# Optimization experiments

Measured on AMD Instinct MI355X. Metric: run time of the kernel, lower is better.

Reference implementation:

```python
import jax, jax.numpy as jnp
import numpy as np

BN_EPS = 1e-5

def _conv1x1(x, W, b):
    # x: (B,C,H,W), W: (O,C) -> (B,O,H,W)
    return jnp.einsum('oc,bchw->bohw', W, x) + b[None, :, None, None]

def setup_inputs() -> dict:
    key = jax.random.key(0)
    ks = jax.random.split(key, 6)
    B, C, H, W = 4, 256, 64, 64
    cq = C // 8
    x  = jax.random.normal(ks[0], (B, C, H, W), jnp.float32)
    Wq = jax.random.normal(ks[1], (cq, C), jnp.float32) * (1.0 / np.sqrt(C))
    Wk = jax.random.normal(ks[2], (cq, C), jnp.float32) * (1.0 / np.sqrt(C))
    Wv = jax.random.normal(ks[3], (C, C), jnp.float32) * (1.0 / np.sqrt(C))
    Wo = jax.random.normal(ks[4], (C, C, 3, 3), jnp.float32) * (1.0 / np.sqrt(C * 9))
    return {
        'x': x,
        'Wq': Wq, 'bq': jnp.zeros((cq,), jnp.float32),
        'Wk': Wk, 'bk': jnp.zeros((cq,), jnp.float32),
        'Wv': Wv, 'bv': jnp.zeros((C,), jnp.float32),
        'Wo': Wo, 'bo': jnp.zeros((C,), jnp.float32),
        'bn_gamma': jnp.ones((C,), jnp.float32),
        'bn_beta':  jnp.zeros((C,), jnp.float32),
        'bn_mean':  jnp.zeros((C,), jnp.float32),
        'bn_var':   jnp.ones((C,), jnp.float32),
    }

def reference(x, Wq, bq, Wk, bk, Wv, bv, Wo, bo, bn_gamma, bn_beta, bn_mean, bn_var):
    B, C, H, W = x.shape
    cq = Wq.shape[0]
    N = H * W
    q = _conv1x1(x, Wq, bq).reshape(B, cq, N)   # (B,cq,N)
    k = _conv1x1(x, Wk, bk).reshape(B, cq, N)   # (B,cq,N)
    v = _conv1x1(x, Wv, bv).reshape(B, C, N)    # (B,C,N)
    scale = cq ** (-0.5)
    attn = jnp.einsum('bcn,bcm->bnm', q, k) * scale   # (B,N,N)
    attn = jax.nn.softmax(attn, axis=-1)
    out = jnp.einsum('bnm,bcm->bcn', attn, v).reshape(B, C, H, W)
    # conv_output: 3x3 conv + BN (inference stats) + ReLU
    out = jax.lax.conv_general_dilated(
        out, Wo, window_strides=(1, 1), padding=((1, 1), (1, 1)),
        dimension_numbers=('NCHW', 'OIHW', 'NCHW')) + bo[None, :, None, None]
    inv = bn_gamma * jax.lax.rsqrt(bn_var + BN_EPS)
    out = out * inv[None, :, None, None] + (bn_beta - bn_mean * inv)[None, :, None, None]
    out = jax.nn.relu(out)
    return out + x
```

## Files before the change

### kernel.cpp

```cpp
#include <hip/hip_runtime.h>
#include <hip/hip_bf16.h>
#include <math.h>

#define N_TOK 4096

typedef __attribute__((ext_vector_type(8))) short short8;
typedef __attribute__((ext_vector_type(4))) float f32x4;

#define MFMA16(a, b, c) __builtin_amdgcn_mfma_f32_16x16x32_bf16(a, b, c, 0, 0, 0)

__device__ inline unsigned pack_bf16x2(float a, float b) {
    __hip_bfloat16 ha = __float2bfloat16(a), hb = __float2bfloat16(b);
    unsigned short ua = *(unsigned short*)&ha, ub = *(unsigned short*)&hb;
    return (unsigned)ua | ((unsigned)ub << 16);
}

__device__ inline float bf2f(unsigned short u) {
    unsigned v = ((unsigned)u) << 16;
    union { unsigned u; float f; } cv; cv.u = v; return cv.f;
}

__device__ inline int swz4(int h, int row) { return (h ^ row ^ (row >> 2)) & 3; }

#define SCK 0.25506974748975505f

__global__ __launch_bounds__(256) void w_prep_kernel(
    const float* __restrict__ Wo, const float* __restrict__ Wq,
    const float* __restrict__ Wk, const float* __restrict__ Wv,
    __hip_bfloat16* __restrict__ Wt, __hip_bfloat16* __restrict__ Wqk,
    __hip_bfloat16* __restrict__ Wvb)
{
    int blk = blockIdx.x, t = threadIdx.x;
    if (blk < 256) {
        const float* src = &Wo[(size_t)(blk * 256 + t) * 9];
#pragma unroll
        for (int tap = 0; tap < 9; ++tap)
            Wt[(size_t)(tap * 256 + blk) * 256 + t] = __float2bfloat16(src[tap]);
    } else if (blk < 260) {
        int r0 = (blk - 256) * 64;
        for (int r = r0; r < r0 + 64; ++r)
            Wvb[r * 256 + t] = __float2bfloat16(Wv[r * 256 + t]);
    } else {
        for (int r = 0; r < 32; ++r) {
            Wqk[r * 256 + t]        = __float2bfloat16(Wq[r * 256 + t] * SCK);
            Wqk[(r + 32) * 256 + t] = __float2bfloat16(Wk[r * 256 + t]);
        }
    }
}

__global__ __launch_bounds__(256) void qkv_kernel(
    const float* __restrict__ x,
    const __hip_bfloat16* __restrict__ Wqk, const __hip_bfloat16* __restrict__ Wvb,
    const float* __restrict__ bq, const float* __restrict__ bk,
    const float* __restrict__ bv,
    __hip_bfloat16* __restrict__ qg, __hip_bfloat16* __restrict__ kg,
    __hip_bfloat16* __restrict__ vg)
{
    __shared__ __hip_bfloat16 tl[32][72];
    int blk = blockIdx.x;
    int b = blk >> 7, n0 = (blk & 127) * 32;
    int t = threadIdx.x, w = t >> 6, lane = t & 63;
    int l15 = lane & 15, l4 = lane >> 4;
    int ns = w & 1, mg = w >> 1;
    int n = n0 + ns * 16 + l15;

    const __hip_bfloat16* wrow[10];
#pragma unroll
    for (int mi = 0; mi < 10; ++mi) {
        int row = mg ? ((6 + mi) * 16 + l15)
                     : (mi < 4 ? (mi * 16 + l15) : 0);
        const __hip_bfloat16* base = mg ? Wvb : (mi < 4 ? Wqk : Wvb);
        if (!mg && mi >= 4) row = (mi - 4) * 16 + l15;
        wrow[mi] = &base[(size_t)row * 256];
    }

    f32x4 zf = {0.f, 0.f, 0.f, 0.f};
    f32x4 acc[10];
#pragma unroll
    for (int m = 0; m < 10; ++m) acc[m] = zf;

    for (int cc = 0; cc < 256; cc += 64) {
        __syncthreads();
#pragma unroll
        for (int rep = 0; rep < 2; ++rep) {
            int c = rep * 32 + (t >> 3);
            int n4 = (t & 7) * 4;
            float4 v4 = *(const float4*)&x[((size_t)(b * 256 + cc + c)) * N_TOK + n0 + n4];
            tl[n4 + 0][c] = __float2bfloat16(v4.x);
            tl[n4 + 1][c] = __float2bfloat16(v4.y);
            tl[n4 + 2][c] = __float2bfloat16(v4.z);
            tl[n4 + 3][c] = __float2bfloat16(v4.w);
        }
        __syncthreads();
#pragma unroll
        for (int kk = 0; kk < 2; ++kk) {
            int k0 = cc + kk * 32;
            short8 bfr = *(const short8*)&tl[ns * 16 + l15][kk * 32 + l4 * 8];
#pragma unroll
            for (int mi = 0; mi < 10; ++mi) {
                short8 af = *(const short8*)&wrow[mi][k0 + l4 * 8];
                acc[mi] = MFMA16(af, bfr, acc[mi]);
            }
        }
    }

    if (mg == 0) {
        f32x4 bq0 = *(const f32x4*)&bq[l4 * 4];
        f32x4 bq1 = *(const f32x4*)&bq[16 + l4 * 4];
        f32x4 bk0 = *(const f32x4*)&bk[l4 * 4];
        f32x4 bk1 = *(const f32x4*)&bk[16 + l4 * 4];
        size_t obase = (size_t)(b * N_TOK + n) * 32;
        uint2 u;
        u.x = pack_bf16x2(acc[0][0] + bq0[0] * SCK, acc[0][1] + bq0[1] * SCK);
        u.y = pack_bf16x2(acc[0][2] + bq0[2] * SCK, acc[0][3] + bq0[3] * SCK);
        *(uint2*)&qg[obase + l4 * 4] = u;
        u.x = pack_bf16x2(acc[1][0] + bq1[0] * SCK, acc[1][1] + bq1[1] * SCK);
        u.y = pack_bf16x2(acc[1][2] + bq1[2] * SCK, acc[1][3] + bq1[3] * SCK);
        *(uint2*)&qg[obase + 16 + l4 * 4] = u;
        u.x = pack_bf16x2(acc[2][0] + bk0[0], acc[2][1] + bk0[1]);
        u.y = pack_bf16x2(acc[2][2] + bk0[2], acc[2][3] + bk0[3]);
        *(uint2*)&kg[obase + l4 * 4] = u;
        u.x = pack_bf16x2(acc[3][0] + bk1[0], acc[3][1] + bk1[1]);
        u.y = pack_bf16x2(acc[3][2] + bk1[2], acc[3][3] + bk1[3]);
        *(uint2*)&kg[obase + 16 + l4 * 4] = u;
#pragma unroll
        for (int mi = 4; mi < 10; ++mi) {
            int cb = (mi - 4) * 16 + l4 * 4;
            f32x4 bvv = *(const f32x4*)&bv[cb];
#pragma unroll
            for (int r = 0; r < 4; ++r)
                vg[((size_t)(b * 256 + cb + r)) * N_TOK + n] = __float2bfloat16(acc[mi][r] + bvv[r]);
        }
    } else {
#pragma unroll
        for (int mi = 0; mi < 10; ++mi) {
            int cb = (6 + mi) * 16 + l4 * 4;
            f32x4 bvv = *(const f32x4*)&bv[cb];
#pragma unroll
            for (int r = 0; r < 4; ++r)
                vg[((size_t)(b * 256 + cb + r)) * N_TOK + n] = __float2bfloat16(acc[mi][r] + bvv[r]);
        }
    }
}

__global__ __launch_bounds__(256, 2) void flash_kernel(
    const __hip_bfloat16* __restrict__ qg, const __hip_bfloat16* __restrict__ kg,
    const __hip_bfloat16* __restrict__ vg,
    __hip_bfloat16* __restrict__ ph0, __hip_bfloat16* __restrict__ ph1,
    float* __restrict__ Lh)
{
    __shared__ __hip_bfloat16 v_lds[2][128 * 64];
    __shared__ __hip_bfloat16 k_lds[2][64 * 32];
    __shared__ __hip_bfloat16 p_lds[4][32 * 64];

    int blk = blockIdx.x;
    int work = (blk & 7) * 64 + (blk >> 3);
    int g = work >> 6;
    int kh = g >> 2, cs = (g >> 1) & 1, bl = g & 1;
    int rem = work & 63;
    int b = ((rem >> 5) << 1) | bl;
    int qgp = rem & 31;
    int t = threadIdx.x, w = t >> 6, lane = t & 63;
    int l15 = lane & 15, l4 = lane >> 4;
    int qw = qgp * 128 + w * 32;

    short8 qf[2];
#pragma unroll
    for (int qs = 0; qs < 2; ++qs)
        qf[qs] = *(const short8*)&qg[((size_t)(b * N_TOK + qw + qs * 16 + l15)) * 32 + l4 * 8];

    f32x4 zf = {0.f, 0.f, 0.f, 0.f};
    f32x4 acc[2][8];
#pragma unroll
    for (int qs = 0; qs < 2; ++qs)
#pragma unroll
        for (int ct = 0; ct < 8; ++ct) acc[qs][ct] = zf;
    float Lr[2] = {0.f, 0.f};

    int vc  = t >> 1;
    int kb4 = (t & 1) * 4;
    int kr  = t >> 2;
    int kch = t & 3;

    const __hip_bfloat16* vrow  = &vg[((size_t)(b * 256 + cs * 128 + vc)) * N_TOK + kh * 2048];
    const __hip_bfloat16* kbase = &kg[((size_t)(b * N_TOK + kh * 2048)) * 32];

    uint4 vp[4], kp;

#pragma unroll
    for (int j = 0; j < 4; ++j)
        vp[j] = *(const uint4*)&vrow[(kb4 + j) * 8];
    kp = *(const uint4*)&kbase[kr * 32 + kch * 8];
#pragma unroll
    for (int j = 0; j < 4; ++j)
        *(uint4*)&v_lds[0][vc * 64 + (((2 * (kb4 + j)) ^ (vc & 14)) << 2)] = vp[j];
    *(uint4*)&k_lds[0][kr * 32 + swz4(kch, kr) * 8] = kp;
    __syncthreads();

    int buf = 0;
    for (int it = 0; it < 32; ++it) {
        int nm0 = it * 64 + 64;
        bool more = (it < 31);
        if (more) {
#pragma unroll
            for (int j = 0; j < 4; ++j)
                vp[j] = *(const uint4*)&vrow[nm0 + (kb4 + j) * 8];
            kp = *(const uint4*)&kbase[(size_t)(nm0 + kr) * 32 + kch * 8];
        }

        short8 kf[4];
#pragma unroll
        for (int kt = 0; kt < 4; ++kt) {
            int row = kt * 16 + l15;
            kf[kt] = *(const short8*)&k_lds[buf][row * 32 + swz4(l4, row) * 8];
        }
        f32x4 sf[2][4];
#pragma unroll
        for (int qs = 0; qs < 2; ++qs)
#pragma unroll
            for (int kt = 0; kt < 4; ++kt)
                sf[qs][kt] = MFMA16(kf[kt], qf[qs], zf);

#pragma unroll
        for (int qs = 0; qs < 2; ++qs) {
            int prow = qs * 16 + l15;
#pragma unroll
            for (int kt = 0; kt < 4; ++kt) {
                float p0 = exp2f(sf[qs][kt][0]);
                float p1 = exp2f(sf[qs][kt][1]);
                float p2 = exp2f(sf[qs][kt][2]);
                float p3 = exp2f(sf[qs][kt][3]);
                Lr[qs] += (p0 + p1) + (p2 + p3);
                uint2 u;
                u.x = pack_bf16x2(p0, p1);
                u.y = pack_bf16x2(p2, p3);
                *(uint2*)&p_lds[w][prow * 64 + (((kt * 4 + l4) ^ (l15 & 14)) << 2)] = u;
            }
        }

#pragma unroll
        for (int ks = 0; ks < 2; ++ks) {
            short8 pb[2];
#pragma unroll
            for (int qs = 0; qs < 2; ++qs)
                pb[qs] = *(const short8*)&p_lds[w][(qs * 16 + l15) * 64 +
                         (((ks * 8 + l4 * 2) ^ (l15 & 14)) << 2)];
#pragma unroll
            for (int ct = 0; ct < 8; ++ct) {
                int cr = ct * 16 + l15;
                short8 vf = *(const short8*)&v_lds[buf][cr * 64 +
                           (((ks * 8 + l4 * 2) ^ (cr & 14)) << 2)];
                acc[0][ct] = MFMA16(vf, pb[0], acc[0][ct]);
                acc[1][ct] = MFMA16(vf, pb[1], acc[1][ct]);
            }
        }

        if (more) {
#pragma unroll
            for (int j = 0; j < 4; ++j)
                *(uint4*)&v_lds[buf ^ 1][vc * 64 + (((2 * (kb4 + j)) ^ (vc & 14)) << 2)] = vp[j];
            *(uint4*)&k_lds[buf ^ 1][kr * 32 + swz4(kch, kr) * 8] = kp;
            buf ^= 1;
        }
        __syncthreads();
    }

#pragma unroll
    for (int qs = 0; qs < 2; ++qs) {
        float L = Lr[qs];
        L += __shfl_xor(L, 16);
        L += __shfl_xor(L, 32);
        int nq = qw + qs * 16 + l15;
        if (cs == 0 && l4 == 0)
            Lh[kh * 16384 + b * 4096 + nq] = L;
        __hip_bfloat16* pdst = kh ? ph1 : ph0;
        size_t pix = (size_t)(b * N_TOK + nq);
#pragma unroll
        for (int ct = 0; ct < 8; ++ct) {
            int cl = cs * 128 + ct * 16 + l4 * 4;
            uint2 u;
            u.x = pack_bf16x2(acc[qs][ct][0], acc[qs][ct][1]);
            u.y = pack_bf16x2(acc[qs][ct][2], acc[qs][ct][3]);
            *(uint2*)&pdst[pix * 256 + cl] = u;
        }
    }
}

__global__ __launch_bounds__(256) void conv_mfma_kernel(
    const __hip_bfloat16* __restrict__ ph0, const __hip_bfloat16* __restrict__ ph1,
    const float* __restrict__ Lh, const __hip_bfloat16* __restrict__ Wt,
    const float* __restrict__ bo,  const float* __restrict__ gamma,
    const float* __restrict__ beta, const float* __restrict__ mean,
    const float* __restrict__ var, const float* __restrict__ x,
    float* __restrict__ out)
{
    __shared__ __hip_bfloat16 in_lds[180 * 32];
    __shared__ __hip_bfloat16 wt_lds[9 * 64 * 32];

    int blk = blockIdx.x;
    int sp = blk & 31, ob = (blk >> 5) & 3, b = blk >> 7;
    int y0 = (sp >> 2) * 8, x0 = (sp & 3) * 16;
    int o0 = ob * 64;
    int t = threadIdx.x;
    int w = t >> 6, lane = t & 63;
    int l15 = lane & 15, l4 = lane >> 4;

    f32x4 zf = {0.f, 0.f, 0.f, 0.f};
    f32x4 acc[4][2];
#pragma unroll
    for (int m = 0; m < 4; ++m)
#pragma unroll
        for (int n = 0; n < 2; ++n) acc[m][n] = zf;

    for (int cc = 0; cc < 256; cc += 32) {
        __syncthreads();
        for (int jj = t; jj < 720; jj += 256) {
            int pix = jj >> 2, h = jj & 3;
            int iy = pix / 18, ix = pix - iy * 18;
            int gy = y0 - 1 + iy, gx = x0 - 1 + ix;
            uint4 val = {0u, 0u, 0u, 0u};
            if (gy >= 0 && gy < 64 && gx >= 0 && gx < 64) {
                int bn = b * 4096 + gy * 64 + gx;
                float inv = 1.f / (Lh[bn] + Lh[16384 + bn]);
                size_t e = (size_t)bn * 256 + cc + h * 8;
                uint4 a  = *(const uint4*)&ph0[e];
                uint4 b4 = *(const uint4*)&ph1[e];
                const unsigned* ap = (const unsigned*)&a;
                const unsigned* bp = (const unsigned*)&b4;
                unsigned* vpn = (unsigned*)&val;
#pragma unroll
                for (int j = 0; j < 4; ++j) {
                    float lo = (bf2f((unsigned short)(ap[j] & 0xffff)) +
                                bf2f((unsigned short)(bp[j] & 0xffff))) * inv;
                    float hi = (bf2f((unsigned short)(ap[j] >> 16)) +
                                bf2f((unsigned short)(bp[j] >> 16))) * inv;
                    vpn[j] = pack_bf16x2(lo, hi);
                }
            }
            *(uint4*)&in_lds[pix * 32 + swz4(h, pix) * 8] = val;
        }
        for (int jj = t; jj < 2304; jj += 256) {
            int tap = jj >> 8, rem = jj & 255;
            int o = rem >> 2, h = rem & 3;
            uint4 wv = *(const uint4*)&Wt[((size_t)(tap * 256 + o0 + o)) * 256 + cc + h * 8];
            *(uint4*)&wt_lds[tap * 2048 + o * 32 + swz4(h, o) * 8] = wv;
        }
        __syncthreads();

#pragma unroll
        for (int ky = 0; ky < 3; ++ky) {
#pragma unroll
            for (int kx = 0; kx < 3; ++kx) {
                int tap = ky * 3 + kx;
                short8 af[4];
#pragma unroll
                for (int m = 0; m < 4; ++m) {
                    int orow = m * 16 + l15;
                    af[m] = *(const short8*)&wt_lds[tap * 2048 + orow * 32 + swz4(l4, orow) * 8];
                }
#pragma unroll
                for (int ntw = 0; ntw < 2; ++ntw) {
                    int yy = w * 2 + ntw;
                    int p = (yy + ky) * 18 + kx + l15;
                    short8 bfr = *(const short8*)&in_lds[p * 32 + swz4(l4, p) * 8];
#pragma unroll
                    for (int m = 0; m < 4; ++m)
                        acc[m][ntw] = MFMA16(af[m], bfr, acc[m][ntw]);
                }
            }
        }
    }

#pragma unroll
    for (int m = 0; m < 4; ++m) {
#pragma unroll
        for (int r = 0; r < 4; ++r) {
            int oc = o0 + m * 16 + l4 * 4 + r;
            float inv = gamma[oc] * rsqrtf(var[oc] + 1e-5f);
            float sh  = (bo[oc] - mean[oc]) * inv + beta[oc];
#pragma unroll
            for (int ntw = 0; ntw < 2; ++ntw) {
                int gy = y0 + w * 2 + ntw, gx = x0 + l15;
                size_t idx = (size_t)(b * 256 + oc) * 4096 + (size_t)gy * 64 + gx;
                float yv = acc[m][ntw][r] * inv + sh;
                yv = fmaxf(yv, 0.f);
                out[idx] = yv + x[idx];
            }
        }
    }
}

extern "C" void kernel_launch(void* const* d_in, const int* in_sizes, int n_in,
                              void* d_out, int out_size, void* d_ws, size_t ws_size,
                              hipStream_t stream)
{
    const float* x  = (const float*)d_in[0];
    const float* Wq = (const float*)d_in[1];
    const float* bq = (const float*)d_in[2];
    const float* Wk = (const float*)d_in[3];
    const float* bk = (const float*)d_in[4];
    const float* Wv = (const float*)d_in[5];
    const float* bv = (const float*)d_in[6];
    const float* Wo = (const float*)d_in[7];
    const float* bo = (const float*)d_in[8];
    const float* gm = (const float*)d_in[9];
    const float* bt = (const float*)d_in[10];
    const float* mn = (const float*)d_in[11];
    const float* vr = (const float*)d_in[12];
    float* out = (float*)d_out;

    char* wsb = (char*)d_ws;
    __hip_bfloat16* qg  = (__hip_bfloat16*)(wsb);
    __hip_bfloat16* kg  = (__hip_bfloat16*)(wsb + (1u  << 20));
    __hip_bfloat16* vg  = (__hip_bfloat16*)(wsb + (2u  << 20));
    __hip_bfloat16* ph1 = (__hip_bfloat16*)(wsb + (10u << 20));
    __hip_bfloat16* Wt  = (__hip_bfloat16*)(wsb + (18u << 20));
    __hip_bfloat16* ph0 = (__hip_bfloat16*)(wsb + (20u << 20));
    __hip_bfloat16* Wqk = (__hip_bfloat16*)(wsb + (28u << 20));
    __hip_bfloat16* Wvb = (__hip_bfloat16*)(wsb + (28u << 20) + 65536);
    float*          Lh  = (float*)(wsb + (28u << 20) + 262144);

    w_prep_kernel  <<<261,  256, 0, stream>>>(Wo, Wq, Wk, Wv, Wt, Wqk, Wvb);
    qkv_kernel     <<<512,  256, 0, stream>>>(x, Wqk, Wvb, bq, bk, bv, qg, kg, vg);
    flash_kernel   <<<512,  256, 0, stream>>>(qg, kg, vg, ph0, ph1, Lh);
    conv_mfma_kernel<<<512, 256, 0, stream>>>(ph0, ph1, Lh, Wt, bo, gm, bt, mn, vr, x, out);
}
```

Measured before the change: 150.0 us.

## Split flash KV range into three chunks and load K fragments directly

The flash attention grid grows from two KV halves to three uneven KV chunks (22/21/21 tiles), giving 768 blocks instead of 512 to spread work more evenly across CUs. K fragments are now loaded from global memory straight into MFMA registers, prefetched one tile ahead, instead of being staged through LDS, which drops the k_lds buffer. The conv kernel then merges three bf16 partial outputs and three row sums, adding a third partial buffer and extra memory traffic in exchange.

```diff
diff --git a/kernel.cpp b/kernel.cpp
--- a/kernel.cpp
+++ b/kernel.cpp
@@ -147,19 +147,18 @@
     const __hip_bfloat16* __restrict__ qg, const __hip_bfloat16* __restrict__ kg,
     const __hip_bfloat16* __restrict__ vg,
     __hip_bfloat16* __restrict__ ph0, __hip_bfloat16* __restrict__ ph1,
-    float* __restrict__ Lh)
+    __hip_bfloat16* __restrict__ ph2, float* __restrict__ Lh)
 {
     __shared__ __hip_bfloat16 v_lds[2][128 * 64];
-    __shared__ __hip_bfloat16 k_lds[2][64 * 32];
     __shared__ __hip_bfloat16 p_lds[4][32 * 64];
 
     int blk = blockIdx.x;
-    int work = (blk & 7) * 64 + (blk >> 3);
-    int g = work >> 6;
-    int kh = g >> 2, cs = (g >> 1) & 1, bl = g & 1;
-    int rem = work & 63;
-    int b = ((rem >> 5) << 1) | bl;
-    int qgp = rem & 31;
+    int work = (blk & 7) * 96 + (blk >> 3);
+    int kh = work >> 8;
+    int rem = work & 255;
+    int cs = rem >> 7, b = (rem >> 5) & 3, qgp = rem & 31;
+    int koff  = (kh == 0) ? 0 : (kh == 1 ? 1408 : 2752);
+    int iters = (kh == 0) ? 22 : 21;
     int t = threadIdx.x, w = t >> 6, lane = t & 63;
     int l15 = lane & 15, l4 = lane >> 4;
     int qw = qgp * 128 + w * 32;
@@ -179,47 +178,43 @@
 
     int vc  = t >> 1;
     int kb4 = (t & 1) * 4;
-    int kr  = t >> 2;
-    int kch = t & 3;
-
-    const __hip_bfloat16* vrow  = &vg[((size_t)(b * 256 + cs * 128 + vc)) * N_TOK + kh * 2048];
-    const __hip_bfloat16* kbase = &kg[((size_t)(b * N_TOK + kh * 2048)) * 32];
-
-    uint4 vp[4], kp;
+
+    const __hip_bfloat16* vrow  = &vg[((size_t)(b * 256 + cs * 128 + vc)) * N_TOK + koff];
+    const __hip_bfloat16* kbase = &kg[((size_t)(b * N_TOK + koff)) * 32];
+
+    uint4 vp[4];
+    short8 kfr[4], kfn[4];
 
 #pragma unroll
     for (int j = 0; j < 4; ++j)
         vp[j] = *(const uint4*)&vrow[(kb4 + j) * 8];
-    kp = *(const uint4*)&kbase[kr * 32 + kch * 8];
+#pragma unroll
+    for (int kt = 0; kt < 4; ++kt)
+        kfr[kt] = *(const short8*)&kbase[(kt * 16 + l15) * 32 + l4 * 8];
 #pragma unroll
     for (int j = 0; j < 4; ++j)
         *(uint4*)&v_lds[0][vc * 64 + (((2 * (kb4 + j)) ^ (vc & 14)) << 2)] = vp[j];
-    *(uint4*)&k_lds[0][kr * 32 + swz4(kch, kr) * 8] = kp;
     __syncthreads();
 
     int buf = 0;
-    for (int it = 0; it < 32; ++it) {
+    for (int it = 0; it < iters; ++it) {
         int nm0 = it * 64 + 64;
-        bool more = (it < 31);
+        bool more = (it < iters - 1);
         if (more) {
 #pragma unroll
             for (int j = 0; j < 4; ++j)
                 vp[j] = *(const uint4*)&vrow[nm0 + (kb4 + j) * 8];
-            kp = *(const uint4*)&kbase[(size_t)(nm0 + kr) * 32 + kch * 8];
-        }
-
-        short8 kf[4];
-#pragma unroll
-        for (int kt = 0; kt < 4; ++kt) {
-            int row = kt * 16 + l15;
-            kf[kt] = *(const short8*)&k_lds[buf][row * 32 + swz4(l4, row) * 8];
-        }
+#pragma unroll
+            for (int kt = 0; kt < 4; ++kt)
+                kfn[kt] = *(const short8*)&kbase[(size_t)(nm0 + kt * 16 + l15) * 32 + l4 * 8];
+        }
+
         f32x4 sf[2][4];
 #pragma unroll
         for (int qs = 0; qs < 2; ++qs)
 #pragma unroll
             for (int kt = 0; kt < 4; ++kt)
-                sf[qs][kt] = MFMA16(kf[kt], qf[qs], zf);
+                sf[qs][kt] = MFMA16(kfr[kt], qf[qs], zf);
 
 #pragma unroll
         for (int qs = 0; qs < 2; ++qs) {
@@ -259,7 +254,8 @@
 #pragma unroll
             for (int j = 0; j < 4; ++j)
                 *(uint4*)&v_lds[buf ^ 1][vc * 64 + (((2 * (kb4 + j)) ^ (vc & 14)) << 2)] = vp[j];
-            *(uint4*)&k_lds[buf ^ 1][kr * 32 + swz4(kch, kr) * 8] = kp;
+#pragma unroll
+            for (int kt = 0; kt < 4; ++kt) kfr[kt] = kfn[kt];
             buf ^= 1;
         }
         __syncthreads();
@@ -273,7 +269,7 @@
         int nq = qw + qs * 16 + l15;
         if (cs == 0 && l4 == 0)
             Lh[kh * 16384 + b * 4096 + nq] = L;
-        __hip_bfloat16* pdst = kh ? ph1 : ph0;
+        __hip_bfloat16* pdst = (kh == 0) ? ph0 : (kh == 1 ? ph1 : ph2);
         size_t pix = (size_t)(b * N_TOK + nq);
 #pragma unroll
         for (int ct = 0; ct < 8; ++ct) {
@@ -288,7 +284,8 @@
 
 __global__ __launch_bounds__(256) void conv_mfma_kernel(
     const __hip_bfloat16* __restrict__ ph0, const __hip_bfloat16* __restrict__ ph1,
-    const float* __restrict__ Lh, const __hip_bfloat16* __restrict__ Wt,
+    const __hip_bfloat16* __restrict__ ph2, const float* __restrict__ Lh,
+    const __hip_bfloat16* __restrict__ Wt,
     const float* __restrict__ bo,  const float* __restrict__ gamma,
     const float* __restrict__ beta, const float* __restrict__ mean,
     const float* __restrict__ var, const float* __restrict__ x,
@@ -321,19 +318,23 @@
             uint4 val = {0u, 0u, 0u, 0u};
             if (gy >= 0 && gy < 64 && gx >= 0 && gx < 64) {
                 int bn = b * 4096 + gy * 64 + gx;
-                float inv = 1.f / (Lh[bn] + Lh[16384 + bn]);
+                float inv = 1.f / (Lh[bn] + Lh[16384 + bn] + Lh[32768 + bn]);
                 size_t e = (size_t)bn * 256 + cc + h * 8;
                 uint4 a  = *(const uint4*)&ph0[e];
                 uint4 b4 = *(const uint4*)&ph1[e];
+                uint4 c4 = *(const uint4*)&ph2[e];
                 const unsigned* ap = (const unsigned*)&a;
                 const unsigned* bp = (const unsigned*)&b4;
+                const unsigned* cp = (const unsigned*)&c4;
                 unsigned* vpn = (unsigned*)&val;
 #pragma unroll
                 for (int j = 0; j < 4; ++j) {
                     float lo = (bf2f((unsigned short)(ap[j] & 0xffff)) +
-                                bf2f((unsigned short)(bp[j] & 0xffff))) * inv;
+                                bf2f((unsigned short)(bp[j] & 0xffff)) +
+                                bf2f((unsigned short)(cp[j] & 0xffff))) * inv;
                     float hi = (bf2f((unsigned short)(ap[j] >> 16)) +
-                                bf2f((unsigned short)(bp[j] >> 16))) * inv;
+                                bf2f((unsigned short)(bp[j] >> 16)) +
+                                bf2f((unsigned short)(cp[j] >> 16))) * inv;
                     vpn[j] = pack_bf16x2(lo, hi);
                 }
             }
@@ -419,9 +420,10 @@
     __hip_bfloat16* Wqk = (__hip_bfloat16*)(wsb + (28u << 20));
     __hip_bfloat16* Wvb = (__hip_bfloat16*)(wsb + (28u << 20) + 65536);
     float*          Lh  = (float*)(wsb + (28u << 20) + 262144);
+    __hip_bfloat16* ph2 = (__hip_bfloat16*)(wsb + (29u << 20));
 
     w_prep_kernel  <<<261,  256, 0, stream>>>(Wo, Wq, Wk, Wv, Wt, Wqk, Wvb);
     qkv_kernel     <<<512,  256, 0, stream>>>(x, Wqk, Wvb, bq, bk, bv, qg, kg, vg);
-    flash_kernel   <<<512,  256, 0, stream>>>(qg, kg, vg, ph0, ph1, Lh);
-    conv_mfma_kernel<<<512, 256, 0, stream>>>(ph0, ph1, Lh, Wt, bo, gm, bt, mn, vr, x, out);
-}
+    flash_kernel   <<<768,  256, 0, stream>>>(qg, kg, vg, ph0, ph1, ph2, Lh);
+    conv_mfma_kernel<<<512, 256, 0, stream>>>(ph0, ph1, ph2, Lh, Wt, bo, gm, bt, mn, vr, x, out);
+}
```

Measured after the change: 174.9 us. 1.17x slower.
